# Kernel optimization log

Hardware: AMD Instinct MI355X
Metric: run time of the kernel (lower is better)

## Reference

```python
import jax, jax.numpy as jnp
import numpy as np

B, S, D, H = 2, 1024, 1024, 16
HD = D // H
WINDOW = 256
FFN = 4 * D


def setup_inputs() -> dict:
    key = jax.random.key(0)
    ks = jax.random.split(key, 12)
    xav = lambda k, o, i: jax.random.normal(k, (o, i), jnp.float32) * np.sqrt(2.0 / (o + i))
    return {
        "x": jax.random.normal(ks[0], (B, S, D), jnp.float32),
        "wq": xav(ks[1], D, D), "bq": jnp.zeros((D,), jnp.float32),
        "wk": xav(ks[2], D, D), "bk": jnp.zeros((D,), jnp.float32),
        "wv": xav(ks[3], D, D), "bv": jnp.zeros((D,), jnp.float32),
        "wo": xav(ks[4], D, D), "bo": jnp.zeros((D,), jnp.float32),
        "attn_norm_w": jnp.ones((D,), jnp.float32),
        "ffn_norm_w": jnp.ones((D,), jnp.float32),
        "gate_w": xav(ks[5], FFN, D),
        "up_w": xav(ks[6], FFN, D),
        "down_w": xav(ks[7], D, FFN),
    }


def _rms(x, w):
    return x * jax.lax.rsqrt(jnp.mean(x * x, axis=-1, keepdims=True) + 1e-6) * w


def _rotate_half(x):
    x1, x2 = jnp.split(x, 2, axis=-1)
    return jnp.concatenate([-x2, x1], axis=-1)


def _rope_cos_sin(seq_len, head_dim):
    inv_freq = 1.0 / (10000.0 ** (jnp.arange(0, head_dim, 2, dtype=jnp.float32) / head_dim))
    freqs = jnp.arange(seq_len, dtype=jnp.float32)[:, None] * inv_freq[None, :]  # [S, HD/2]
    emb = jnp.concatenate([freqs, freqs], axis=-1)  # [S, HD]
    return jnp.cos(emb)[None, None], jnp.sin(emb)[None, None]  # [1,1,S,HD]


def reference(x, wq, bq, wk, bk, wv, bv, wo, bo, attn_norm_w, ffn_norm_w, gate_w, up_w, down_w):
    b, s, d = x.shape
    scale = 1.0 / np.sqrt(HD)
    residual = x
    h = _rms(x, attn_norm_w)
    q = (h @ wq.T + bq).reshape(b, s, H, HD).transpose(0, 2, 1, 3)  # [B,H,S,HD]
    k = (h @ wk.T + bk).reshape(b, s, H, HD).transpose(0, 2, 1, 3)
    v = (h @ wv.T + bv).reshape(b, s, H, HD).transpose(0, 2, 1, 3)
    cos, sin = _rope_cos_sin(s, HD)
    q = q * cos + _rotate_half(q) * sin
    k = k * cos + _rotate_half(k) * sin
    scores = jnp.einsum("bhqd,bhkd->bhqk", q, k) * scale  # dense [B,H,S,S]
    i = jnp.arange(s)[:, None]
    j = jnp.arange(s)[None, :]
    local_mask = (j <= i) & (i - j < WINDOW)  # causal sliding window
    scores = jnp.where(local_mask[None, None], scores, -jnp.inf)
    attn = jax.nn.softmax(scores, axis=-1)
    out = jnp.einsum("bhqk,bhkd->bhqd", attn, v)
    out = out.transpose(0, 2, 1, 3).reshape(b, s, d) @ wo.T + bo
    x = residual + out
    residual = x
    h = _rms(x, ffn_norm_w)
    ffn = (jax.nn.silu(h @ gate_w.T) * (h @ up_w.T)) @ down_w.T
    return (residual + ffn, attn)
```

## Files before the change

### kernel.cpp

```cpp
#include <hip/hip_runtime.h>

typedef unsigned short u16;
typedef unsigned int u32;
typedef __attribute__((ext_vector_type(8))) short short8;
typedef __attribute__((ext_vector_type(4))) float f32x4;

__device__ __forceinline__ float b2fu(u32 u) {
  union { u32 i; float f; } v; v.i = u << 16; return v.f;
}
__device__ __forceinline__ u16 f2bu(float f) {
  union { float f; u32 i; } v; v.f = f;
  u32 r = (v.i + 0x7fffu + ((v.i >> 16) & 1u)) >> 16;
  return (u16)r;
}
__device__ __forceinline__ void gl_lds16(const void* g, void* l) {
  __builtin_amdgcn_global_load_lds((const __attribute__((address_space(1))) void*)g,
                                   (__attribute__((address_space(3))) void*)l, 16, 0, 0);
}
__device__ __forceinline__ short8 ld_lds_b8(const u16* p) {
  uint2 a = *(const uint2*)p;
  uint2 b = *(const uint2*)(p + 4);
  union { u32 u[4]; short8 s; } v;
  v.u[0] = a.x; v.u[1] = a.y; v.u[2] = b.x; v.u[3] = b.y;
  return v.s;
}

__global__ __launch_bounds__(256) void cvt_weights(
    const float* __restrict__ wq, const float* __restrict__ wk,
    const float* __restrict__ wv, const float* __restrict__ wo,
    const float* __restrict__ wg, const float* __restrict__ wu,
    const float* __restrict__ wd, u16* __restrict__ dst,
    const float* __restrict__ bq, const float* __restrict__ bk,
    const float* __restrict__ bv, float* __restrict__ bqkv)
{
  if (blockIdx.x >= 16384) {
    const int s = blockIdx.x - 16384;
    const float* bsrc = (s == 0) ? bq : (s == 1) ? bk : bv;
    const int o = threadIdx.x * 4;
    *(float4*)(bqkv + s * 1024 + o) = *(const float4*)(bsrc + o);
    return;
  }
  size_t e = ((size_t)blockIdx.x * 256 + threadIdx.x) * 4;
  size_t seg = e >> 20;
  const float* src; size_t soff;
  if      (seg == 0) { src = wq; soff = e; }
  else if (seg == 1) { src = wk; soff = e - ((size_t)1 << 20); }
  else if (seg == 2) { src = wv; soff = e - ((size_t)2 << 20); }
  else if (seg == 3) { src = wo; soff = e - ((size_t)3 << 20); }
  else if (seg < 12) {
    size_t idx = e - ((size_t)4 << 20);
    int rc = (int)(idx >> 10);
    int col = (int)(idx & 1023);
    int bi = rc >> 5, j = rc & 31;
    if (j < 16) { src = wg; soff = (size_t)(bi * 16 + j) * 1024 + col; }
    else        { src = wu; soff = (size_t)(bi * 16 + j - 16) * 1024 + col; }
  }
  else { src = wd; soff = e - ((size_t)12 << 20); }
  float4 v = *(const float4*)(src + soff);
  *(ushort4*)(dst + e) = make_ushort4(f2bu(v.x), f2bu(v.y), f2bu(v.z), f2bu(v.w));
}

__global__ __launch_bounds__(256) void rmsnorm_kernel(
    const float* __restrict__ x, const float* __restrict__ w, u16* __restrict__ out)
{
  const int row = blockIdx.x;
  const int t = threadIdx.x;
  float4 v = ((const float4*)(x + (size_t)row * 1024))[t];
  float ss = v.x * v.x + v.y * v.y + v.z * v.z + v.w * v.w;
#pragma unroll
  for (int m = 32; m > 0; m >>= 1) ss += __shfl_xor(ss, m, 64);
  __shared__ float red[4];
  if ((t & 63) == 0) red[t >> 6] = ss;
  __syncthreads();
  float tot = red[0] + red[1] + red[2] + red[3];
  float r = rsqrtf(tot * (1.0f / 1024.0f) + 1e-6f);
  float4 wv = ((const float4*)w)[t];
  ushort4 o = make_ushort4(f2bu(v.x * r * wv.x), f2bu(v.y * r * wv.y),
                           f2bu(v.z * r * wv.z), f2bu(v.w * r * wv.w));
  ((ushort4*)(out + (size_t)row * 1024))[t] = o;
}

template<int TMB, int TNB, int EPI, bool HAS_BIAS, bool HAS_RES, bool SPLIT>
__global__ __launch_bounds__(256) void gemm_bt(
    const u16* __restrict__ A, const u16* __restrict__ B, float* __restrict__ C,
    const float* __restrict__ bias, const float* __restrict__ res,
    int M, int N, int K, int lda,
    u16* __restrict__ P0, u16* __restrict__ P1, u16* __restrict__ P2)
{
  constexpr int BK = 32;
  constexpr int WTM = TMB / 2, WTN = TNB / 2;
  constexpr int MT = WTM / 16, NT = WTN / 16;
  __shared__ u16 As[TMB * BK];
  __shared__ u16 Bs[TNB * BK];
  const int t = threadIdx.x;
  const int w = t >> 6, l = t & 63;
  const int wm = (w >> 1) * WTM, wn = (w & 1) * WTN;
  const int lr = l & 15, lq = l >> 4;
  const int tile_m = blockIdx.y * TMB, tile_n = blockIdx.x * TNB;
  const int kb = SPLIT ? blockIdx.z * K : 0;
  if (SPLIT) C += (size_t)blockIdx.z * M * N;

  f32x4 acc[MT][NT] = {};

  const int sr = t >> 2;
  const int scs = (((t & 3) ^ ((t >> 3) & 3)) * 8);
  const int rsw = (lq ^ ((lr >> 1) & 3)) * 8;
  const u16* Ab = A + (size_t)(tile_m + sr) * lda + kb + scs;
  const u16* Bb = B + (size_t)(tile_n + sr) * lda + kb + scs;

  for (int kk = 0; kk < K; kk += BK) {
#pragma unroll
    for (int i = 0; i < TMB / 64; ++i)
      gl_lds16(Ab + kk + (size_t)i * 64 * lda, &As[t * 8 + i * 2048]);
#pragma unroll
    for (int i = 0; i < TNB / 64; ++i)
      gl_lds16(Bb + kk + (size_t)i * 64 * lda, &Bs[t * 8 + i * 2048]);
    __syncthreads();
    short8 af[MT], bfr[NT];
#pragma unroll
    for (int mt = 0; mt < MT; ++mt)
      af[mt] = *(const short8*)&As[(wm + mt * 16 + lr) * BK + rsw];
#pragma unroll
    for (int nt = 0; nt < NT; ++nt)
      bfr[nt] = *(const short8*)&Bs[(wn + nt * 16 + lr) * BK + rsw];
#pragma unroll
    for (int mt = 0; mt < MT; ++mt)
#pragma unroll
      for (int nt = 0; nt < NT; ++nt)
        acc[mt][nt] = __builtin_amdgcn_mfma_f32_16x16x32_bf16(af[mt], bfr[nt], acc[mt][nt], 0, 0, 0);
    __syncthreads();
  }

  if (EPI == 0) {
#pragma unroll
    for (int nt = 0; nt < NT; ++nt) {
      const int col = tile_n + wn + nt * 16 + lr;
      const float bv = HAS_BIAS ? bias[col] : 0.0f;
#pragma unroll
      for (int mt = 0; mt < MT; ++mt) {
        const int row0 = tile_m + wm + mt * 16 + lq * 4;
#pragma unroll
        for (int r = 0; r < 4; ++r) {
          const size_t off = (size_t)(row0 + r) * N + col;
          float v = acc[mt][nt][r] + bv;
          if (HAS_RES) v += res[off];
          C[off] = v;
        }
      }
    }
  } else if (EPI == 1) {
    const int colbase = tile_n + wn;
    const int seg = colbase >> 10;
    const int h = (colbase >> 6) & 15;
    u16* dstb = (seg == 0) ? P0 : (seg == 1) ? P1 : P2;
    float bv[NT];
#pragma unroll
    for (int nt = 0; nt < NT; ++nt) bv[nt] = bias[colbase + nt * 16 + lr];
#pragma unroll
    for (int mt = 0; mt < MT; ++mt) {
      const int row0 = tile_m + wm + mt * 16 + lq * 4;
#pragma unroll
      for (int r = 0; r < 4; ++r) {
        const int row = row0 + r;
        const int s = row & 1023, b = row >> 10;
        u16* dst = dstb + (((size_t)(b * 16 + h) << 10) + s) * 64;
        if (seg < 2) {
#pragma unroll
          for (int np = 0; np < 2; ++np) {
            const int i = np * 16 + lr;
            const float th = (float)s * exp2f(-0.4152410118609203f * (float)i);
            float sn, cs; __sincosf(th, &sn, &cs);
            const float g0 = acc[mt][np][r] + bv[np];
            const float g2 = acc[mt][np + 2][r] + bv[np + 2];
            dst[i]      = f2bu(g0 * cs - g2 * sn);
            dst[i + 32] = f2bu(g2 * cs + g0 * sn);
          }
        } else {
#pragma unroll
          for (int nt = 0; nt < NT; ++nt)
            dst[nt * 16 + lr] = f2bu(acc[mt][nt][r] + bv[nt]);
        }
      }
    }
  } else {
#pragma unroll
    for (int nt = 0; nt < NT; nt += 2) {
      const int feat = (((tile_n + wn + nt * 16) >> 5) << 4) + lr;
#pragma unroll
      for (int mt = 0; mt < MT; ++mt) {
        const int row0 = tile_m + wm + mt * 16 + lq * 4;
#pragma unroll
        for (int r = 0; r < 4; ++r) {
          const float g = acc[mt][nt][r];
          const float u = acc[mt][nt + 1][r];
          const float a = g / (1.0f + __expf(-g)) * u;
          P0[(size_t)(row0 + r) * (N >> 1) + feat] = f2bu(a);
        }
      }
    }
  }
}

#define FPH(buf, kk, mth, dostage, dovm) do {                                                  \
    if ((mth) == 0) {                                                                          \
      _Pragma("unroll")                                                                        \
      for (int nt = 0; nt < 4; ++nt)                                                           \
        bfr[nt] = *(const short8*)&Bs[(buf) * 16384 + (wn + nt * 16 + lr) * 64 +               \
                                      (((kk) * 32 + lq * 8) ^ cxor)];                          \
    }                                                                                          \
    short8 af[4];                                                                              \
    _Pragma("unroll")                                                                          \
    for (int mt = 0; mt < 4; ++mt)                                                             \
      af[mt] = *(const short8*)&As[(buf) * 16384 + (wm + (mth) * 64 + mt * 16 + lr) * 64 +     \
                                   (((kk) * 32 + lq * 8) ^ cxor)];                             \
    if (dostage) STAGE_ALL(kt + 1);                                                            \
    __builtin_amdgcn_s_barrier();                                                              \
    asm volatile("s_waitcnt lgkmcnt(0)" ::: "memory");                                         \
    __builtin_amdgcn_sched_barrier(0);                                                         \
    __builtin_amdgcn_s_setprio(1);                                                             \
    _Pragma("unroll")                                                                          \
    for (int mt = 0; mt < 4; ++mt)                                                             \
      _Pragma("unroll")                                                                        \
      for (int nt = 0; nt < 4; ++nt)                                                           \
        acc[(mth) * 4 + mt][nt] =                                                              \
            __builtin_amdgcn_mfma_f32_16x16x32_bf16(af[mt], bfr[nt], acc[(mth) * 4 + mt][nt],  \
                                                    0, 0, 0);                                  \
    __builtin_amdgcn_s_setprio(0);                                                             \
    if (dovm) asm volatile("s_waitcnt vmcnt(0)" ::: "memory");                                 \
    __builtin_amdgcn_s_barrier();                                                              \
  } while (0)

__global__ __launch_bounds__(512, 2) void ffn1_8ph(
    const u16* __restrict__ A, const u16* __restrict__ B, u16* __restrict__ act)
{
  __shared__ u16 As[32768];
  __shared__ u16 Bs[32768];
  const int t = threadIdx.x;
  const int wid = t >> 6, l = t & 63;
  const int lr = l & 15, lq = l >> 4;
  const int wm = (wid >> 2) * 128, wn = (wid & 3) * 64;
  const int tile_m = blockIdx.y * 256, tile_n = blockIdx.x * 256;
  const int cxor = (lr & 7) * 8;

  const int srow = t >> 3;
  const int schunk = (t & 7) ^ (srow & 7);
  const u16* aRow = A + (size_t)(tile_m + srow) * 1024 + schunk * 8;
  const u16* bRow = B + (size_t)(tile_n + srow) * 1024 + schunk * 8;

  auto STAGE_ALL = [&](int kt2) {
    if (kt2 < 16) {
      const int bz2 = kt2 & 1;
      const u16* ga = aRow + kt2 * 64;
      const u16* gb = bRow + kt2 * 64;
      u16* da = As + bz2 * 16384 + t * 8;
      u16* db = Bs + bz2 * 16384 + t * 8;
      gl_lds16(ga, da);
      gl_lds16(ga + 64 * 1024, da + 4096);
      gl_lds16(ga + 128 * 1024, da + 8192);
      gl_lds16(ga + 192 * 1024, da + 12288);
      gl_lds16(gb, db);
      gl_lds16(gb + 64 * 1024, db + 4096);
      gl_lds16(gb + 128 * 1024, db + 8192);
      gl_lds16(gb + 192 * 1024, db + 12288);
    }
  };

  f32x4 acc[8][4] = {};
  short8 bfr[4];

  STAGE_ALL(0);
  asm volatile("s_waitcnt vmcnt(0)" ::: "memory");
  __builtin_amdgcn_s_barrier();

  for (int kt = 0; kt < 16; ++kt) {
    const int bz = kt & 1;
    FPH(bz, 0, 0, 1, 0);
    FPH(bz, 0, 1, 0, 0);
    FPH(bz, 1, 0, 0, 0);
    FPH(bz, 1, 1, 0, 1);
  }

#pragma unroll
  for (int nt = 0; nt < 4; nt += 2) {
    const int feat = (((tile_n + wn + nt * 16) >> 5) << 4) + lr;
#pragma unroll
    for (int mi = 0; mi < 8; ++mi) {
      const int row0 = tile_m + wm + mi * 16 + lq * 4;
#pragma unroll
      for (int r = 0; r < 4; ++r) {
        const float g = acc[mi][nt][r];
        const float u = acc[mi][nt + 1][r];
        const float a = g / (1.0f + __expf(-g)) * u;
        act[(size_t)(row0 + r) * 4096 + feat] = f2bu(a);
      }
    }
  }
}

__global__ __launch_bounds__(256) void reduce4_kernel(
    const float* __restrict__ p, const float* __restrict__ res, float* __restrict__ out)
{
  const size_t i = ((size_t)blockIdx.x * 256 + threadIdx.x) * 4;
  float4 a = *(const float4*)(p + i);
  float4 b = *(const float4*)(p + i + 2097152);
  float4 c = *(const float4*)(p + i + 2 * 2097152);
  float4 d = *(const float4*)(p + i + 3 * 2097152);
  float4 r = *(const float4*)(res + i);
  float4 o;
  o.x = r.x + a.x + b.x + c.x + d.x;
  o.y = r.y + a.y + b.y + c.y + d.y;
  o.z = r.z + a.z + b.z + c.z + d.z;
  o.w = r.w + a.w + b.w + c.w + d.w;
  *(float4*)(out + i) = o;
}

#define KP 68
#define PP 292

__global__ __launch_bounds__(256) void attn_kernel(
    const u16* __restrict__ qb, const u16* __restrict__ kb, const u16* __restrict__ vb,
    float* __restrict__ probs, u16* __restrict__ ctx)
{
  __shared__ u16 Kbuf[288 * KP];
  __shared__ u16 Vbuf[288 * KP];
  __shared__ float smax[2][32];
  __shared__ float ssum[2][32];
  u16* Pbuf = Kbuf;

  const int blk = blockIdx.x;
  const int qt = blk & 31, bh = blk >> 5;
  const int b = bh >> 4, h = bh & 15;
  const int q0 = qt << 5;
  const int kstart = (q0 > 255) ? (q0 - 255) : 0;
  const int span = q0 + 32 - kstart;
  const int t = threadIdx.x;
  const int w = t >> 6, l = t & 63;
  const int lr = l & 15, lq = l >> 4;
  const int mw = w & 1, nh = w >> 1;
  const size_t bhS = (size_t)bh << 10;

  {
    const u16* kg = kb + ((bhS + (size_t)kstart) << 6);
    const u16* vg = vb + ((bhS + (size_t)kstart) << 6);
    for (int idx = t; idx < 288 * 8; idx += 256) {
      const int r = idx >> 3, c = (idx & 7) << 3;
      uint4 kv4 = make_uint4(0, 0, 0, 0), vv4 = make_uint4(0, 0, 0, 0);
      if (r < span) {
        kv4 = *(const uint4*)&kg[(r << 6) + c];
        vv4 = *(const uint4*)&vg[(r << 6) + c];
      }
      *(uint2*)&Kbuf[r * KP + c]     = make_uint2(kv4.x, kv4.y);
      *(uint2*)&Kbuf[r * KP + c + 4] = make_uint2(kv4.z, kv4.w);
      *(uint2*)&Vbuf[r * KP + c]     = make_uint2(vv4.x, vv4.y);
      *(uint2*)&Vbuf[r * KP + c + 4] = make_uint2(vv4.z, vv4.w);
    }
  }
  short8 qa0, qa1;
  {
    const u16* qrow = qb + ((bhS + (size_t)(q0 + mw * 16 + lr)) << 6) + lq * 8;
    qa0 = *(const short8*)qrow;
    qa1 = *(const short8*)(qrow + 32);
  }
  __syncthreads();

  f32x4 acc[9];
#pragma unroll
  for (int i = 0; i < 9; ++i) acc[i] = (f32x4){0.f, 0.f, 0.f, 0.f};
#pragma unroll
  for (int i = 0; i < 9; ++i) {
    const int nt = nh + 2 * i;
    const u16* kr = &Kbuf[(nt * 16 + lr) * KP + lq * 8];
    short8 kf0 = ld_lds_b8(kr);
    short8 kf1 = ld_lds_b8(kr + 32);
    acc[i] = __builtin_amdgcn_mfma_f32_16x16x32_bf16(qa0, kf0, acc[i], 0, 0, 0);
    acc[i] = __builtin_amdgcn_mfma_f32_16x16x32_bf16(qa1, kf1, acc[i], 0, 0, 0);
  }

  const int rbase = mw * 16 + lq * 4;
  float rmax[4] = {-1e30f, -1e30f, -1e30f, -1e30f};
#pragma unroll
  for (int i = 0; i < 9; ++i) {
    const int jg = kstart + (nh + 2 * i) * 16 + lr;
#pragma unroll
    for (int r = 0; r < 4; ++r) {
      const int q = q0 + rbase + r;
      const bool valid = (jg >= q - 255) && (jg <= q);
      const float v = valid ? acc[i][r] * 0.125f : -1e30f;
      acc[i][r] = v;
      rmax[r] = fmaxf(rmax[r], v);
    }
  }
#pragma unroll
  for (int r = 0; r < 4; ++r) {
    float m_ = rmax[r];
    m_ = fmaxf(m_, __shfl_xor(m_, 1, 64));
    m_ = fmaxf(m_, __shfl_xor(m_, 2, 64));
    m_ = fmaxf(m_, __shfl_xor(m_, 4, 64));
    m_ = fmaxf(m_, __shfl_xor(m_, 8, 64));
    rmax[r] = m_;
  }
  if (lr == 0) {
#pragma unroll
    for (int r = 0; r < 4; ++r) smax[nh][rbase + r] = rmax[r];
  }
  __syncthreads();
#pragma unroll
  for (int r = 0; r < 4; ++r)
    rmax[r] = fmaxf(smax[0][rbase + r], smax[1][rbase + r]);
  float rsum[4] = {0.f, 0.f, 0.f, 0.f};
#pragma unroll
  for (int i = 0; i < 9; ++i)
#pragma unroll
    for (int r = 0; r < 4; ++r) {
      const float p = exp2f((acc[i][r] - rmax[r]) * 1.44269504f);
      acc[i][r] = p;
      rsum[r] += p;
    }
#pragma unroll
  for (int r = 0; r < 4; ++r) {
    float s_ = rsum[r];
    s_ += __shfl_xor(s_, 1, 64);
    s_ += __shfl_xor(s_, 2, 64);
    s_ += __shfl_xor(s_, 4, 64);
    s_ += __shfl_xor(s_, 8, 64);
    rsum[r] = s_;
  }
  if (lr == 0) {
#pragma unroll
    for (int r = 0; r < 4; ++r) ssum[nh][rbase + r] = rsum[r];
  }
  __syncthreads();

  float inv4[4];
#pragma unroll
  for (int r = 0; r < 4; ++r)
    inv4[r] = 1.0f / (ssum[0][rbase + r] + ssum[1][rbase + r]);
#pragma unroll
  for (int i = 0; i < 9; ++i) {
    const int nt = nh + 2 * i;
#pragma unroll
    for (int r = 0; r < 4; ++r)
      Pbuf[(rbase + r) * PP + nt * 16 + lr] = f2bu(acc[i][r] * inv4[r]);
  }
  __syncthreads();

  {
    const int row = t >> 3;
    const int q = q0 + row;
    const int c0 = (t & 7) << 7;
    const int lo = q - 255;
    float* prow = probs + ((bhS + (size_t)q) << 10) + c0;
    const u16* pr = &Pbuf[row * PP];
#pragma unroll 4
    for (int cc = 0; cc < 128; cc += 4) {
      const int c = c0 + cc;
      float4 o;
      o.x = (c + 0 >= lo && c + 0 <= q) ? b2fu(pr[c + 0 - kstart]) : 0.0f;
      o.y = (c + 1 >= lo && c + 1 <= q) ? b2fu(pr[c + 1 - kstart]) : 0.0f;
      o.z = (c + 2 >= lo && c + 2 <= q) ? b2fu(pr[c + 2 - kstart]) : 0.0f;
      o.w = (c + 3 >= lo && c + 3 <= q) ? b2fu(pr[c + 3 - kstart]) : 0.0f;
      *(float4*)&prow[cc] = o;
    }
  }

  const int n0 = (w >> 1) * 2;
  f32x4 oacc[2] = {};
#pragma unroll
  for (int ks = 0; ks < 9; ++ks) {
    short8 pa = ld_lds_b8(&Pbuf[(mw * 16 + lr) * PP + ks * 32 + lq * 8]);
#pragma unroll
    for (int nn = 0; nn < 2; ++nn) {
      const int d = (n0 + nn) * 16 + lr;
      union { u16 u[8]; short8 s; } bf_;
#pragma unroll
      for (int jj = 0; jj < 8; ++jj)
        bf_.u[jj] = Vbuf[(ks * 32 + lq * 8 + jj) * KP + d];
      oacc[nn] = __builtin_amdgcn_mfma_f32_16x16x32_bf16(pa, bf_.s, oacc[nn], 0, 0, 0);
    }
  }
#pragma unroll
  for (int nn = 0; nn < 2; ++nn) {
    const int d = (n0 + nn) * 16 + lr;
#pragma unroll
    for (int r = 0; r < 4; ++r) {
      const int q = q0 + rbase + r;
      ctx[(((size_t)(b * 1024 + q)) << 10) + (h << 6) + d] = f2bu(oacc[nn][r]);
    }
  }
}

extern "C" void kernel_launch(void* const* d_in, const int* in_sizes, int n_in,
                              void* d_out, int out_size, void* d_ws, size_t ws_size,
                              hipStream_t stream) {
  (void)in_sizes; (void)n_in; (void)out_size; (void)ws_size;
  const float* x   = (const float*)d_in[0];
  const float* wq  = (const float*)d_in[1];
  const float* bq  = (const float*)d_in[2];
  const float* wk  = (const float*)d_in[3];
  const float* bk  = (const float*)d_in[4];
  const float* wv  = (const float*)d_in[5];
  const float* bv  = (const float*)d_in[6];
  const float* wo  = (const float*)d_in[7];
  const float* bo  = (const float*)d_in[8];
  const float* anw = (const float*)d_in[9];
  const float* fnw = (const float*)d_in[10];
  const float* wg  = (const float*)d_in[11];
  const float* wu  = (const float*)d_in[12];
  const float* wd  = (const float*)d_in[13];

  char* ws = (char*)d_ws;
  u16*   wbf  = (u16*)ws;
  float* bqkv = (float*)(ws + ((size_t)32 << 20));
  u16*   h1   = (u16*)(ws + ((size_t)32 << 20) + (16 << 10));
  char*  R    = ws + ((size_t)36 << 20) + (16 << 10);
  u16*   qbp  = (u16*)R;
  u16*   kbp  = (u16*)(R + ((size_t)4 << 20));
  u16*   vbp  = (u16*)(R + ((size_t)8 << 20));
  u16*   ctx  = (u16*)(R + ((size_t)12 << 20));
  float* x1   = (float*)(R + ((size_t)16 << 20));
  u16*   h2   = (u16*)(R + ((size_t)24 << 20));
  u16*   act  = (u16*)(R + ((size_t)28 << 20));
  float* pbuf = (float*)(R + ((size_t)44 << 20));

  float* out0  = (float*)d_out;
  float* probs = (float*)d_out + 2097152;

  cvt_weights<<<16387, 256, 0, stream>>>(wq, wk, wv, wo, wg, wu, wd, wbf,
                                          bq, bk, bv, bqkv);

  rmsnorm_kernel<<<2048, 256, 0, stream>>>(x, anw, h1);
  gemm_bt<128, 128, 1, true, false, false><<<dim3(24, 16), 256, 0, stream>>>(
      h1, wbf, nullptr, bqkv, nullptr, 2048, 3072, 1024, 1024, qbp, kbp, vbp);
  attn_kernel<<<1024, 256, 0, stream>>>(qbp, kbp, vbp, probs, ctx);
  gemm_bt<64, 128, 0, true, true, false><<<dim3(8, 32), 256, 0, stream>>>(
      ctx, wbf + ((size_t)3 << 20), x1, bo, x, 2048, 1024, 1024, 1024,
      nullptr, nullptr, nullptr);

  rmsnorm_kernel<<<2048, 256, 0, stream>>>(x1, fnw, h2);
  ffn1_8ph<<<dim3(32, 8), 512, 0, stream>>>(h2, wbf + ((size_t)4 << 20), act);
  gemm_bt<128, 128, 0, false, false, true><<<dim3(8, 16, 4), 256, 0, stream>>>(
      act, wbf + ((size_t)12 << 20), pbuf, nullptr, nullptr, 2048, 1024, 1024, 4096,
      nullptr, nullptr, nullptr);
  reduce4_kernel<<<2048, 256, 0, stream>>>(pbuf, x1, out0);
}
```

Measured before the change: 410.5 us.

## Replace down-projection GEMM with 256x256 8-phase split-K kernel

The FFN down projection moves from the generic 128x128 split-K-4 GEMM to a dedicated 512-thread kernel. It uses 256x256 tiles, direct global-to-LDS loads, double buffering and the FPH phase macro reused from ffn1. Split-K rises to 8 (256 blocks total) and the reduction kernel now sums 8 partials plus the residual. Larger tiles cut global reloads and give better MFMA reuse, at the cost of more partial-buffer traffic in the reduce step and higher LDS and register use.

```diff
diff --git a/kernel.cpp b/kernel.cpp
--- a/kernel.cpp
+++ b/kernel.cpp
@@ -297,20 +297,81 @@
   }
 }
 
-__global__ __launch_bounds__(256) void reduce4_kernel(
+__global__ __launch_bounds__(512, 2) void down_8ph(
+    const u16* __restrict__ A, const u16* __restrict__ B, float* __restrict__ C)
+{
+  __shared__ u16 As[32768];
+  __shared__ u16 Bs[32768];
+  const int t = threadIdx.x;
+  const int wid = t >> 6, l = t & 63;
+  const int lr = l & 15, lq = l >> 4;
+  const int wm = (wid >> 2) * 128, wn = (wid & 3) * 64;
+  const int tile_m = blockIdx.y * 256, tile_n = blockIdx.x * 256;
+  const int kb = blockIdx.z * 512;
+  const int cxor = (lr & 7) * 8;
+
+  const int srow = t >> 3;
+  const int schunk = (t & 7) ^ (srow & 7);
+  const u16* aRow = A + (size_t)(tile_m + srow) * 4096 + kb + schunk * 8;
+  const u16* bRow = B + (size_t)(tile_n + srow) * 4096 + kb + schunk * 8;
+
+  auto STAGE_ALL = [&](int kt2) {
+    if (kt2 < 8) {
+      const int bz2 = kt2 & 1;
+      const u16* ga = aRow + kt2 * 64;
+      const u16* gb = bRow + kt2 * 64;
+      u16* da = As + bz2 * 16384 + t * 8;
+      u16* db = Bs + bz2 * 16384 + t * 8;
+      gl_lds16(ga, da);
+      gl_lds16(ga + (size_t)64 * 4096, da + 4096);
+      gl_lds16(ga + (size_t)128 * 4096, da + 8192);
+      gl_lds16(ga + (size_t)192 * 4096, da + 12288);
+      gl_lds16(gb, db);
+      gl_lds16(gb + (size_t)64 * 4096, db + 4096);
+      gl_lds16(gb + (size_t)128 * 4096, db + 8192);
+      gl_lds16(gb + (size_t)192 * 4096, db + 12288);
+    }
+  };
+
+  f32x4 acc[8][4] = {};
+  short8 bfr[4];
+
+  STAGE_ALL(0);
+  asm volatile("s_waitcnt vmcnt(0)" ::: "memory");
+  __builtin_amdgcn_s_barrier();
+
+  for (int kt = 0; kt < 8; ++kt) {
+    const int bz = kt & 1;
+    FPH(bz, 0, 0, 1, 0);
+    FPH(bz, 0, 1, 0, 0);
+    FPH(bz, 1, 0, 0, 0);
+    FPH(bz, 1, 1, 0, 1);
+  }
+
+  float* Cp = C + (size_t)blockIdx.z * 2048 * 1024;
+#pragma unroll
+  for (int nt = 0; nt < 4; ++nt) {
+    const int col = tile_n + wn + nt * 16 + lr;
+#pragma unroll
+    for (int mi = 0; mi < 8; ++mi) {
+      const int row0 = tile_m + wm + mi * 16 + lq * 4;
+#pragma unroll
+      for (int r = 0; r < 4; ++r)
+        Cp[(size_t)(row0 + r) * 1024 + col] = acc[mi][nt][r];
+    }
+  }
+}
+
+__global__ __launch_bounds__(256) void reduce8_kernel(
     const float* __restrict__ p, const float* __restrict__ res, float* __restrict__ out)
 {
   const size_t i = ((size_t)blockIdx.x * 256 + threadIdx.x) * 4;
-  float4 a = *(const float4*)(p + i);
-  float4 b = *(const float4*)(p + i + 2097152);
-  float4 c = *(const float4*)(p + i + 2 * 2097152);
-  float4 d = *(const float4*)(p + i + 3 * 2097152);
-  float4 r = *(const float4*)(res + i);
-  float4 o;
-  o.x = r.x + a.x + b.x + c.x + d.x;
-  o.y = r.y + a.y + b.y + c.y + d.y;
-  o.z = r.z + a.z + b.z + c.z + d.z;
-  o.w = r.w + a.w + b.w + c.w + d.w;
+  float4 o = *(const float4*)(res + i);
+#pragma unroll
+  for (int z = 0; z < 8; ++z) {
+    float4 a = *(const float4*)(p + i + (size_t)z * 2097152);
+    o.x += a.x; o.y += a.y; o.z += a.z; o.w += a.w;
+  }
   *(float4*)(out + i) = o;
 }
 
@@ -538,8 +599,6 @@
 
   rmsnorm_kernel<<<2048, 256, 0, stream>>>(x1, fnw, h2);
   ffn1_8ph<<<dim3(32, 8), 512, 0, stream>>>(h2, wbf + ((size_t)4 << 20), act);
-  gemm_bt<128, 128, 0, false, false, true><<<dim3(8, 16, 4), 256, 0, stream>>>(
-      act, wbf + ((size_t)12 << 20), pbuf, nullptr, nullptr, 2048, 1024, 1024, 4096,
-      nullptr, nullptr, nullptr);
-  reduce4_kernel<<<2048, 256, 0, stream>>>(pbuf, x1, out0);
-}
+  down_8ph<<<dim3(4, 8, 8), 512, 0, stream>>>(act, wbf + ((size_t)12 << 20), pbuf);
+  reduce8_kernel<<<2048, 256, 0, stream>>>(pbuf, x1, out0);
+}
```

Result: no change. 418.7 us (+2.0%).
